# Kernel optimization log

Hardware: AMD Instinct MI355X
Metric: run time of the kernel (lower is better)

Reference implementation:

```python
import jax, jax.numpy as jnp
import numpy as np
from jax import lax

NC = 32
EPS = 1e-12


def unfold3x3(x):
    # x: [B,C,H,W] -> [B, C*9, H*W], matching F.unfold(kernel=3, padding=1)
    B, C, H, W = x.shape
    xp = jnp.pad(x, ((0, 0), (0, 0), (1, 1), (1, 1)))
    patches = jnp.stack([xp[:, :, i:i + H, j:j + W]
                         for i in range(3) for j in range(3)], axis=2)  # [B,C,9,H,W]
    return patches.reshape(B, C * 9, H * W)


def fold3x3(u, H, W):
    # u: [B, C*9, H*W] -> [B, C, H, W], matching F.fold(kernel=3, padding=1)
    B = u.shape[0]
    C = u.shape[1] // 9
    p = u.reshape(B, C, 3, 3, H, W)
    out = jnp.zeros((B, C, H + 2, W + 2), u.dtype)
    for i in range(3):
        for j in range(3):
            out = out.at[:, :, i:i + H, j:j + W].add(p[:, :, i, j])
    return out[:, :, 1:H + 1, 1:W + 1]


def l2norm(x, axis):
    n = jnp.sqrt(jnp.sum(x * x, axis=axis, keepdims=True))
    return x / jnp.maximum(n, EPS)


def conv3x3(x, w, b):
    y = lax.conv_general_dilated(x, w, (1, 1), 'SAME',
                                 dimension_numbers=('NCHW', 'OIHW', 'NCHW'))
    return y + b[None, :, None, None]


def setup_inputs() -> dict:
    key = jax.random.key(0)
    k = jax.random.split(key, 6)
    B, C, H, W = 2, NC, 80, 80
    in_HSI = jax.random.normal(k[0], (B, C, H, W), jnp.float32)
    in_PAN = jax.random.normal(k[1], (B, C, H, W), jnp.float32)
    fan1 = 2 * C * 9
    fan2 = C * 9
    w1 = jax.random.normal(k[2], (C, 2 * C, 3, 3), jnp.float32) / np.sqrt(fan1)
    b1 = jax.random.normal(k[3], (C,), jnp.float32) * 0.01
    w2 = jax.random.normal(k[4], (C, C, 3, 3), jnp.float32) / np.sqrt(fan2)
    b2 = jax.random.normal(k[5], (C,), jnp.float32) * 0.01
    return {"in_HSI": in_HSI, "in_PAN": in_PAN, "w1": w1, "b1": b1, "w2": w2, "b2": b2}


def reference(in_HSI, in_PAN, w1, b1, w2, b2):
    B, C, H, W = in_HSI.shape
    L = H * W
    HSI_unfold = unfold3x3(in_HSI)                      # [B, C*9, L]
    PAN_unfold = unfold3x3(in_PAN)                      # [B, C*9, L]
    PAN_q = l2norm(jnp.transpose(PAN_unfold, (0, 2, 1)), axis=2)  # [B, L, C*9]
    HSI_k = l2norm(HSI_unfold, axis=1)                  # [B, C*9, L]
    R = jnp.einsum('blc,bcm->blm', PAN_q, HSI_k)        # [B, L, L]
    R_star = jnp.max(R, axis=1)                         # [B, L]
    R_arg = jnp.argmax(R, axis=1)                       # [B, L]
    # gather columns of unfold(in_PAN) selected by 1-NN indices
    T_unfold = jnp.take_along_axis(PAN_unfold, R_arg[:, None, :], axis=2)
    T_lv3 = fold3x3(T_unfold, H, W) / 9.0               # [B, C, H, W]
    S = R_star.reshape(B, 1, H, W)
    h = jax.nn.relu(conv3x3(jnp.concatenate([T_lv3, in_HSI], axis=1), w1, b1))
    res = conv3x3(h, w2, b2) * S + in_HSI
    return res
```

## Files before the change

kernel.cpp:

```cpp
#include <hip/hip_runtime.h>
#include <hip/hip_bf16.h>
#include <hip/hip_fp16.h>
#include <stdint.h>

#define HH 80
#define WW 80
#define LL 6400
#define CC 32
#define BB 2
#define COG 8
#define DELTA 0.011f
#define NT8 800

typedef __bf16 bf16x8 __attribute__((ext_vector_type(8)));
typedef float  f32x4  __attribute__((ext_vector_type(4)));

__device__ __forceinline__ int div80(int v) {
    return (int)(((unsigned)v * 52429u) >> 22);
}

__device__ __forceinline__ unsigned short f2bf(float f) {
    unsigned int u = __float_as_uint(f);
    return (unsigned short)((u + 0x7fffu + ((u >> 16) & 1u)) >> 16);
}

__global__ __launch_bounds__(256) void fusedunf_kernel(const float* __restrict__ HSI,
                                                       const float* __restrict__ PAN,
                                                       float* __restrict__ invH,
                                                       float* __restrict__ invP,
                                                       float* __restrict__ PANunf,
                                                       float* __restrict__ HSIunf,
                                                       char* __restrict__ Apack,
                                                       char* __restrict__ Bpack) {
    __shared__ float simg[CC][3][82];
    __shared__ float sinv[80];
    const int y = blockIdx.x, mat = blockIdx.y, b = blockIdx.z;
    const int tid = threadIdx.x;
    const float* img = (mat ? HSI : PAN) + (size_t)b * CC * LL;

    for (int i = tid; i < CC * 3; i += 256) {
        simg[i / 3][i % 3][0] = 0.f;
        simg[i / 3][i % 3][81] = 0.f;
    }
    for (int i = tid; i < CC * 3 * 80; i += 256) {
        int c = i / 240, r = i - c * 240;
        int dy = r / 80, x = r - dy * 80;
        int yy = y + dy - 1;
        float v = ((unsigned)yy < 80u) ? img[(size_t)c * LL + yy * 80 + x] : 0.f;
        simg[c][dy][x + 1] = v;
    }
    __syncthreads();

    if (tid < 80) {
        float s = 0.f;
        #pragma unroll 4
        for (int c = 0; c < CC; ++c)
            #pragma unroll
            for (int dy = 0; dy < 3; ++dy)
                #pragma unroll
                for (int dx = 0; dx < 3; ++dx) {
                    float v = simg[c][dy][tid + dx];
                    s = fmaf(v, v, s);
                }
        float inv = 1.f / fmaxf(sqrtf(s), 1e-12f);
        sinv[tid] = inv;
        (mat ? invH : invP)[b * LL + y * 80 + tid] = inv;
    }
    __syncthreads();

    {
        float* unfBase = (mat ? HSIunf : PANunf) + ((size_t)b * LL + y * 80) * 288;
        for (int i = tid; i < 5760; i += 256) {
            const int fidx = i * 4;
            const int l = fidx / 288, k = fidx - l * 288;
            float4 v;
            {
                int kk = k;     int c = kk / 9, t = kk - c * 9; v.x = simg[c][t / 3][l + t % 3];
                kk = k + 1;     c = kk / 9; t = kk - c * 9;     v.y = simg[c][t / 3][l + t % 3];
                kk = k + 2;     c = kk / 9; t = kk - c * 9;     v.z = simg[c][t / 3][l + t % 3];
                kk = k + 3;     c = kk / 9; t = kk - c * 9;     v.w = simg[c][t / 3][l + t % 3];
            }
            *(float4*)(unfBase + fidx) = v;
        }
    }

    {
        char* pk = mat ? Bpack : Apack;
        for (int i = tid; i < 2880; i += 256) {
            const int l = i / 36, g = i - l * 36;
            const float inv = sinv[l];
            unsigned short hs[8];
            #pragma unroll
            for (int jj = 0; jj < 8; ++jj) {
                int kk = g * 8 + jj;
                int c = kk / 9, t = kk - c * 9;
                hs[jj] = f2bf(simg[c][t / 3][l + t % 3] * inv);
            }
            const int q = g / 12;
            const int slot = (g % 12) ^ (l & 15);
            size_t off = ((size_t)(b * 3 + q) * LL + y * 80 + l) * 256 + slot * 16;
            uint4 hv;
            hv.x = hs[0] | ((unsigned)hs[1] << 16); hv.y = hs[2] | ((unsigned)hs[3] << 16);
            hv.z = hs[4] | ((unsigned)hs[5] << 16); hv.w = hs[6] | ((unsigned)hs[7] << 16);
            *(uint4*)(pk + off) = hv;
        }
    }
}

__global__ __launch_bounds__(256, 2) void simq_kernel(const char* __restrict__ Apack,
                                                      const char* __restrict__ Bpack,
                                                      __half* __restrict__ tileMax8,
                                                      __half* __restrict__ tileMax64) {
    const int orig = blockIdx.x;
    const int xcd = orig & 7, idx = orig >> 3;
    const int wg = (xcd < 4 ? xcd * 63 : 252 + (xcd - 4) * 62) + idx;
    const int b = wg / 250;
    int rest = wg - b * 250;
    const int sp = rest / 50;
    const int mt = rest - sp * 50;

    const int tid = threadIdx.x;
    const int lane = tid & 63, w = tid >> 6;
    const int wl = w >> 1, wm = w & 1;
    const int r15 = lane & 15, h = lane >> 4;
    const char* Ab = Apack + (size_t)b * 3 * LL * 256;
    const char* Bb = Bpack + (size_t)b * 3 * LL * 256;
    const int m0 = mt * 128;
    const f32x4 fzero = {0.f, 0.f, 0.f, 0.f};

    int gp[3];
    #pragma unroll
    for (int ks = 0; ks < 3; ++ks) gp[ks] = ((ks * 4 + h) ^ r15) * 16;

    bf16x8 bq[3][3][4];
    {
        const int rowb = m0 + wm * 64 + r15;
        #pragma unroll
        for (int c = 0; c < 3; ++c)
            #pragma unroll
            for (int ks = 0; ks < 3; ++ks)
                #pragma unroll
                for (int fm = 0; fm < 4; ++fm)
                    bq[c][ks][fm] = *(const bf16x8*)(Bb + ((size_t)c * LL + rowb + fm * 16) * 256 + gp[ks]);
    }

    const char* Abase = Ab + (size_t)(wl * 64 + r15) * 256;

    #pragma unroll 1
    for (int lt = 0; lt < 10; ++lt) {
        const int l0 = (sp * 10 + lt) * 128;
        const char* Alt = Abase + (size_t)l0 * 256;
        f32x4 acc[4][4];
        #pragma unroll
        for (int i = 0; i < 4; ++i)
            #pragma unroll
            for (int j = 0; j < 4; ++j) acc[i][j] = fzero;

        #pragma unroll
        for (int c = 0; c < 3; ++c) {
            #pragma unroll
            for (int ks = 0; ks < 3; ++ks) {
                bf16x8 af[4];
                #pragma unroll
                for (int f = 0; f < 4; ++f)
                    af[f] = *(const bf16x8*)(Alt + ((size_t)c * LL + f * 16) * 256 + gp[ks]);
                #pragma unroll
                for (int fl = 0; fl < 4; ++fl)
                    #pragma unroll
                    for (int fm = 0; fm < 4; ++fm)
                        acc[fl][fm] = __builtin_amdgcn_mfma_f32_16x16x32_bf16(
                            af[fl], bq[c][ks][fm], acc[fl][fm], 0, 0, 0);
            }
        }

        const int T64 = (sp * 10 + lt) * 2 + wl;
        #pragma unroll
        for (int fm = 0; fm < 4; ++fm) {
            float m4[4];
            #pragma unroll
            for (int fl = 0; fl < 4; ++fl) {
                f32x4 a = acc[fl][fm];
                m4[fl] = fmaxf(fmaxf(a[0], a[1]), fmaxf(a[2], a[3]));
            }
            const int m = m0 + wm * 64 + fm * 16 + r15;
            #pragma unroll
            for (int fl = 0; fl < 4; ++fl) {
                float v = fmaxf(m4[fl], __shfl_xor(m4[fl], 16, 64));
                if ((h & 1) == 0)
                    tileMax8[((size_t)b * LL + m) * NT8 + T64 * 8 + fl * 2 + (h >> 1)] = __float2half(v);
            }
            float vA = fmaxf(fmaxf(m4[0], m4[1]), fmaxf(m4[2], m4[3]));
            vA = fmaxf(vA, __shfl_xor(vA, 16, 64));
            vA = fmaxf(vA, __shfl_xor(vA, 32, 64));
            if (h == 0)
                tileMax64[((size_t)b * LL + m) * 100 + T64] = __float2half(vA);
        }
    }
}

__global__ __launch_bounds__(256) void scanfix_kernel(const float* __restrict__ PANunf,
                                                      const float* __restrict__ HSIunf,
                                                      const float* __restrict__ invH,
                                                      const float* __restrict__ invP,
                                                      const __half* __restrict__ tileMax8,
                                                      const __half* __restrict__ tileMax64,
                                                      float* __restrict__ Sv, int* __restrict__ Sa) {
    const int orig = blockIdx.x;
    const int swz = (orig & 7) * 400 + (orig >> 3);
    const int gw = swz * 4 + (threadIdx.x >> 6);
    const int lane = threadIdx.x & 63;
    const int b = gw / LL;
    const __half* tm64 = tileMax64 + (size_t)gw * 100;
    const __half* tm8  = tileMax8  + (size_t)gw * NT8;

    float t64[2];
    #pragma unroll
    for (int i = 0; i < 2; ++i) {
        int T = i * 64 + lane;
        t64[i] = (T < 100) ? __half2float(tm64[T]) : -3.0e38f;
    }
    float v1 = fmaxf(t64[0], t64[1]);
    #pragma unroll
    for (int d = 1; d < 64; d <<= 1) v1 = fmaxf(v1, __shfl_xor(v1, d, 64));
    const float th = v1 - DELTA;

    const float ihm = invH[gw];
    const int lql = lane >> 3, kq = lane & 7;

    float hreg[36];
    {
        const float4* hv4 = (const float4*)(HSIunf + (size_t)gw * 288 + kq * 36);
        #pragma unroll
        for (int j = 0; j < 9; ++j) {
            float4 v = hv4[j];
            hreg[j * 4 + 0] = v.x; hreg[j * 4 + 1] = v.y;
            hreg[j * 4 + 2] = v.z; hreg[j * 4 + 3] = v.w;
        }
    }

    float bv = -3.0e38f; int bl = 0x7fffffff;

    #pragma unroll 1
    for (int i = 0; i < 2; ++i) {
        unsigned long long mask = __ballot(t64[i] >= th);
        while (mask) {
            const int t = __ffsll((long long)mask) - 1;
            mask &= mask - 1;
            const int T64 = i * 64 + t;
            float s8 = __half2float(tm8[T64 * 8 + (lane & 7)]);
            unsigned sub = (unsigned)(__ballot(s8 >= th) & 0xffull);
            while (sub) {
                const int j = __ffs(sub) - 1;
                sub &= sub - 1;
                const int T = T64 * 8 + j;
                const int l = T * 8 + lql;
                const float4* pv4 = (const float4*)(PANunf + ((size_t)b * LL + l) * 288 + kq * 36);
                float part = 0.f;
                #pragma unroll
                for (int jj = 0; jj < 9; ++jj) {
                    float4 p = pv4[jj];
                    part = fmaf(p.x, hreg[jj * 4 + 0], part);
                    part = fmaf(p.y, hreg[jj * 4 + 1], part);
                    part = fmaf(p.z, hreg[jj * 4 + 2], part);
                    part = fmaf(p.w, hreg[jj * 4 + 3], part);
                }
                part += __shfl_xor(part, 1, 64);
                part += __shfl_xor(part, 2, 64);
                part += __shfl_xor(part, 4, 64);
                const float val = part * invP[b * LL + l] * ihm;
                if (val > bv || (val == bv && l < bl)) { bv = val; bl = l; }
            }
        }
    }
    #pragma unroll
    for (int d = 1; d < 64; d <<= 1) {
        float ov = __shfl_xor(bv, d, 64);
        int   ol = __shfl_xor(bl, d, 64);
        if (ov > bv || (ov == bv && ol < bl)) { bv = ov; bl = ol; }
    }
    if (lane == 0) { Sv[gw] = bv; Sa[gw] = bl; }
}

__global__ void tfold_kernel(const float* __restrict__ PAN, const int* __restrict__ Sa,
                             float* __restrict__ T) {
    int g = blockIdx.x * blockDim.x + threadIdx.x;
    if (g >= BB * CC * LL) return;
    int bc = g / LL, l = g - bc * LL;
    int b = bc >> 5;
    int y = div80(l), x = l - y * 80;
    const float* img = PAN + (size_t)bc * LL;
    const int* Sab = Sa + b * LL;
    float acc = 0.f;
    #pragma unroll
    for (int i = 0; i < 3; ++i) {
        int yp = y + 1 - i;
        if ((unsigned)yp >= 80u) continue;
        #pragma unroll
        for (int j = 0; j < 3; ++j) {
            int xp = x + 1 - j;
            if ((unsigned)xp >= 80u) continue;
            int a = Sab[yp * 80 + xp];
            int ya = div80(a), xa = a - ya * 80;
            int py = ya + i - 1, px = xa + j - 1;
            if ((unsigned)py < 80u && (unsigned)px < 80u) acc += img[py * 80 + px];
        }
    }
    T[g] = acc * (1.f / 9.f);
}

__global__ __launch_bounds__(256) void conv1_kernel(const float* __restrict__ T,
                                                    const float* __restrict__ HSI,
                                                    const float* __restrict__ w1,
                                                    const float* __restrict__ b1,
                                                    float* __restrict__ h) {
    __shared__ __align__(16) float wl[64][9][COG];
    const int tid = threadIdx.x;
    const int co0 = blockIdx.y * COG;
    for (int idx = tid; idx < 64 * 9 * COG; idx += 256) {
        int cog = idx & (COG - 1);
        int rest = idx >> 3;
        int cin = rest / 9, tap = rest - cin * 9;
        wl[cin][tap][cog] = w1[(co0 + cog) * (64 * 9) + cin * 9 + tap];
    }
    __syncthreads();
    const int g = blockIdx.x * 256 + tid;
    const int b = g / LL, l = g - b * LL;
    const int y = div80(l), x = l - y * 80;
    float acc[COG];
    #pragma unroll
    for (int i = 0; i < COG; ++i) acc[i] = 0.f;
    for (int cin = 0; cin < 64; ++cin) {
        const float* img = (cin < CC) ? (T + (size_t)(b * CC + cin) * LL)
                                      : (HSI + (size_t)(b * CC + (cin - CC)) * LL);
        float tap[9];
        #pragma unroll
        for (int i = 0; i < 3; ++i)
            #pragma unroll
            for (int j = 0; j < 3; ++j) {
                int yy = y + i - 1, xx = x + j - 1;
                tap[i * 3 + j] = ((unsigned)yy < 80u && (unsigned)xx < 80u) ? img[yy * 80 + xx] : 0.f;
            }
        #pragma unroll
        for (int t9 = 0; t9 < 9; ++t9) {
            const float4 wa = *reinterpret_cast<const float4*>(&wl[cin][t9][0]);
            const float4 wb = *reinterpret_cast<const float4*>(&wl[cin][t9][4]);
            acc[0] = fmaf(tap[t9], wa.x, acc[0]);
            acc[1] = fmaf(tap[t9], wa.y, acc[1]);
            acc[2] = fmaf(tap[t9], wa.z, acc[2]);
            acc[3] = fmaf(tap[t9], wa.w, acc[3]);
            acc[4] = fmaf(tap[t9], wb.x, acc[4]);
            acc[5] = fmaf(tap[t9], wb.y, acc[5]);
            acc[6] = fmaf(tap[t9], wb.z, acc[6]);
            acc[7] = fmaf(tap[t9], wb.w, acc[7]);
        }
    }
    #pragma unroll
    for (int cog = 0; cog < COG; ++cog) {
        float v = acc[cog] + b1[co0 + cog];
        h[(size_t)(b * CC + co0 + cog) * LL + l] = fmaxf(v, 0.f);
    }
}

__global__ __launch_bounds__(256) void conv2_kernel(const float* __restrict__ hbuf,
                                                    const float* __restrict__ HSI,
                                                    const float* __restrict__ Sv,
                                                    const float* __restrict__ w2,
                                                    const float* __restrict__ b2,
                                                    float* __restrict__ out) {
    __shared__ __align__(16) float wl[CC][9][COG];
    const int tid = threadIdx.x;
    const int co0 = blockIdx.y * COG;
    for (int idx = tid; idx < CC * 9 * COG; idx += 256) {
        int cog = idx & (COG - 1);
        int rest = idx >> 3;
        int cin = rest / 9, tap = rest - cin * 9;
        wl[cin][tap][cog] = w2[(co0 + cog) * (CC * 9) + cin * 9 + tap];
    }
    __syncthreads();
    const int g = blockIdx.x * 256 + tid;
    const int b = g / LL, l = g - b * LL;
    const int y = div80(l), x = l - y * 80;
    float acc[COG];
    #pragma unroll
    for (int i = 0; i < COG; ++i) acc[i] = 0.f;
    for (int cin = 0; cin < CC; ++cin) {
        const float* img = hbuf + (size_t)(b * CC + cin) * LL;
        float tap[9];
        #pragma unroll
        for (int i = 0; i < 3; ++i)
            #pragma unroll
            for (int j = 0; j < 3; ++j) {
                int yy = y + i - 1, xx = x + j - 1;
                tap[i * 3 + j] = ((unsigned)yy < 80u && (unsigned)xx < 80u) ? img[yy * 80 + xx] : 0.f;
            }
        #pragma unroll
        for (int t9 = 0; t9 < 9; ++t9) {
            const float4 wa = *reinterpret_cast<const float4*>(&wl[cin][t9][0]);
            const float4 wb = *reinterpret_cast<const float4*>(&wl[cin][t9][4]);
            acc[0] = fmaf(tap[t9], wa.x, acc[0]);
            acc[1] = fmaf(tap[t9], wa.y, acc[1]);
            acc[2] = fmaf(tap[t9], wa.z, acc[2]);
            acc[3] = fmaf(tap[t9], wa.w, acc[3]);
            acc[4] = fmaf(tap[t9], wb.x, acc[4]);
            acc[5] = fmaf(tap[t9], wb.y, acc[5]);
            acc[6] = fmaf(tap[t9], wb.z, acc[6]);
            acc[7] = fmaf(tap[t9], wb.w, acc[7]);
        }
    }
    const float s = Sv[b * LL + l];
    #pragma unroll
    for (int cog = 0; cog < COG; ++cog) {
        int c = co0 + cog;
        out[(size_t)(b * CC + c) * LL + l] = fmaf(acc[cog] + b2[c], s, HSI[(size_t)(b * CC + c) * LL + l]);
    }
}

extern "C" void kernel_launch(void* const* d_in, const int* in_sizes, int n_in,
                              void* d_out, int out_size, void* d_ws, size_t ws_size,
                              hipStream_t stream) {
    const float* HSI = (const float*)d_in[0];
    const float* PAN = (const float*)d_in[1];
    const float* w1  = (const float*)d_in[2];
    const float* b1  = (const float*)d_in[3];
    const float* w2  = (const float*)d_in[4];
    const float* b2  = (const float*)d_in[5];
    float* out = (float*)d_out;

    char* ws = (char*)d_ws;
    size_t off = 0;
    auto alloc = [&](size_t bytes) -> void* {
        void* p = ws + off;
        off += (bytes + 255) & ~(size_t)255;
        return p;
    };
    float* invH  = (float*)alloc((size_t)BB * LL * 4);
    float* invP  = (float*)alloc((size_t)BB * LL * 4);
    char*  Apack = (char*) alloc((size_t)BB * 3 * LL * 256);
    char*  Bpack = (char*) alloc((size_t)BB * 3 * LL * 256);
    __half* tileMax8  = (__half*)alloc((size_t)BB * LL * NT8 * 2);
    __half* tileMax64 = (__half*)alloc((size_t)BB * LL * 100 * 2);
    float* PANunf = (float*)alloc((size_t)BB * LL * 288 * 4);
    float* HSIunf = (float*)alloc((size_t)BB * LL * 288 * 4);
    float* Sv    = (float*)alloc((size_t)BB * LL * 4);
    int*   Sa    = (int*)  alloc((size_t)BB * LL * 4);
    float* T     = (float*)alloc((size_t)BB * CC * LL * 4);
    float* hbuf  = (float*)alloc((size_t)BB * CC * LL * 4);

    fusedunf_kernel<<<dim3(80, 2, BB), 256, 0, stream>>>(HSI, PAN, invH, invP,
                                                         PANunf, HSIunf, Apack, Bpack);
    simq_kernel<<<dim3(500), 256, 0, stream>>>(Apack, Bpack, tileMax8, tileMax64);
    scanfix_kernel<<<dim3(BB * LL / 4), 256, 0, stream>>>(PANunf, HSIunf, invH, invP,
                                                          tileMax8, tileMax64, Sv, Sa);
    tfold_kernel<<<dim3((BB * CC * LL + 255) / 256), 256, 0, stream>>>(PAN, Sa, T);
    conv1_kernel<<<dim3(BB * LL / 256, CC / COG), 256, 0, stream>>>(T, HSI, w1, b1, hbuf);
    conv2_kernel<<<dim3(BB * LL / 256, CC / COG), 256, 0, stream>>>(hbuf, HSI, Sv, w2, b2, out);
}
```

Baseline: 272.6 us.

## Stage similarity GEMM operands in LDS with double-buffered async global loads

The similarity kernel used to keep the whole B operand in registers and read A fragments straight from global memory. It now copies the 128-row B block into LDS once, and streams A tiles into a double-buffered LDS area with global_load_lds, prefetching the next channel slice while the MFMAs consume the current one. This should cut register pressure and overlap global latency with compute. The cost is about 160KB of LDS per block, occupancy dropping to one block per CU, and two barriers per slice.

```diff
diff --git a/kernel.cpp b/kernel.cpp
--- a/kernel.cpp
+++ b/kernel.cpp
@@ -22,6 +22,12 @@
 __device__ __forceinline__ unsigned short f2bf(float f) {
     unsigned int u = __float_as_uint(f);
     return (unsigned short)((u + 0x7fffu + ((u >> 16) & 1u)) >> 16);
+}
+
+__device__ __forceinline__ void gload_lds16(const void* g, void* l) {
+    __builtin_amdgcn_global_load_lds(
+        (const __attribute__((address_space(1))) void*)g,
+        (__attribute__((address_space(3))) void*)l, 16, 0, 0);
 }
 
 __global__ __launch_bounds__(256) void fusedunf_kernel(const float* __restrict__ HSI,
@@ -107,10 +113,12 @@
     }
 }
 
-__global__ __launch_bounds__(256, 2) void simq_kernel(const char* __restrict__ Apack,
+__global__ __launch_bounds__(256, 1) void simq_kernel(const char* __restrict__ Apack,
                                                       const char* __restrict__ Bpack,
                                                       __half* __restrict__ tileMax8,
                                                       __half* __restrict__ tileMax64) {
+    __shared__ __align__(16) char Alds[2][32768];
+    __shared__ __align__(16) char Blds[98304];
     const int orig = blockIdx.x;
     const int xcd = orig & 7, idx = orig >> 3;
     const int wg = (xcd < 4 ? xcd * 63 : 252 + (xcd - 4) * 62) + idx;
@@ -132,24 +140,29 @@
     #pragma unroll
     for (int ks = 0; ks < 3; ++ks) gp[ks] = ((ks * 4 + h) ^ r15) * 16;
 
-    bf16x8 bq[3][3][4];
+    #pragma unroll 1
+    for (int it = 0; it < 24; ++it) {
+        const int i = it * 256 + tid;
+        const int pl = i >> 11;
+        const int off = (i & 2047) * 16;
+        gload_lds16(Bb + ((size_t)pl * LL + m0) * 256 + off, Blds + i * 16);
+    }
+
+    const char* gAbase = Ab + w * 8192 + lane * 16;
+    char* lA0 = Alds[0] + w * 8192;
+    char* lA1 = Alds[1] + w * 8192;
+
     {
-        const int rowb = m0 + wm * 64 + r15;
-        #pragma unroll
-        for (int c = 0; c < 3; ++c)
-            #pragma unroll
-            for (int ks = 0; ks < 3; ++ks)
-                #pragma unroll
-                for (int fm = 0; fm < 4; ++fm)
-                    bq[c][ks][fm] = *(const bf16x8*)(Bb + ((size_t)c * LL + rowb + fm * 16) * 256 + gp[ks]);
-    }
-
-    const char* Abase = Ab + (size_t)(wl * 64 + r15) * 256;
-
+        const char* gA = gAbase + ((size_t)(sp * 10) * 128) * 256;
+        #pragma unroll
+        for (int i = 0; i < 8; ++i) gload_lds16(gA + i * 1024, lA0 + i * 1024);
+    }
+
+    const char* Bw = Blds + (wm * 64 + r15) * 256;
+    int cur = 0;
     #pragma unroll 1
     for (int lt = 0; lt < 10; ++lt) {
         const int l0 = (sp * 10 + lt) * 128;
-        const char* Alt = Abase + (size_t)l0 * 256;
         f32x4 acc[4][4];
         #pragma unroll
         for (int i = 0; i < 4; ++i)
@@ -158,19 +171,40 @@
 
         #pragma unroll
         for (int c = 0; c < 3; ++c) {
+            if (c < 2 || lt < 9) {
+                const int c2  = (c + 1) % 3;
+                const int l0n = (c == 2) ? l0 + 128 : l0;
+                const char* gA = gAbase + ((size_t)c2 * LL + l0n) * 256;
+                char* lA = (cur ^ 1) ? lA1 : lA0;
+                #pragma unroll
+                for (int i = 0; i < 8; ++i) gload_lds16(gA + i * 1024, lA + i * 1024);
+                asm volatile("s_waitcnt vmcnt(8)" ::: "memory");
+            } else {
+                asm volatile("s_waitcnt vmcnt(0)" ::: "memory");
+            }
+            __builtin_amdgcn_s_barrier();
+            asm volatile("" ::: "memory");
+            const char* lAr = Alds[cur];
+            const char* lBc = Bw + c * 32768;
             #pragma unroll
             for (int ks = 0; ks < 3; ++ks) {
-                bf16x8 af[4];
+                bf16x8 af[4], bfr[4];
                 #pragma unroll
-                for (int f = 0; f < 4; ++f)
-                    af[f] = *(const bf16x8*)(Alt + ((size_t)c * LL + f * 16) * 256 + gp[ks]);
+                for (int f = 0; f < 4; ++f) {
+                    af[f]  = *(const bf16x8*)(lAr + (wl * 64 + f * 16 + r15) * 256 + gp[ks]);
+                    bfr[f] = *(const bf16x8*)(lBc + (f * 16) * 256 + gp[ks]);
+                }
                 #pragma unroll
                 for (int fl = 0; fl < 4; ++fl)
                     #pragma unroll
                     for (int fm = 0; fm < 4; ++fm)
                         acc[fl][fm] = __builtin_amdgcn_mfma_f32_16x16x32_bf16(
-                            af[fl], bq[c][ks][fm], acc[fl][fm], 0, 0, 0);
-            }
+                            af[fl], bfr[fm], acc[fl][fm], 0, 0, 0);
+            }
+            asm volatile("s_waitcnt lgkmcnt(0)" ::: "memory");
+            __builtin_amdgcn_s_barrier();
+            asm volatile("" ::: "memory");
+            cur ^= 1;
         }
 
         const int T64 = (sp * 10 + lt) * 2 + wl;
```

Measured after the change: 255.5 us. -6.3%, faster.
